# Kernel tuning notes

Hardware: AMD Instinct MI355X
Metric: run time of the kernel (lower is better)

## Reference

```python
import jax, jax.numpy as jnp
import numpy as np

B = 131072
MV_IN, PC_IN, D, OUT = 256, 128, 128, 128
LN_EPS = 1e-5
NORM_EPS = 1e-9


def _lin_init(key, fan_in, fan_out):
    kw, kb = jax.random.split(key)
    s = 1.0 / np.sqrt(fan_in)
    W = jax.random.uniform(kw, (fan_in, fan_out), minval=-s, maxval=s, dtype=jnp.float32)
    b = jax.random.uniform(kb, (fan_out,), minval=-s, maxval=s, dtype=jnp.float32)
    return W, b


def setup_inputs() -> dict:
    key = jax.random.key(0)
    ks = jax.random.split(key, 12)
    mv_enc = jax.random.normal(ks[0], (B, MV_IN), dtype=jnp.float32)
    pc_enc = jax.random.normal(ks[1], (B, PC_IN), dtype=jnp.float32)
    Wq_mv, bq_mv = _lin_init(ks[2], MV_IN, D)
    Wk_mv, bk_mv = _lin_init(ks[3], MV_IN, D)
    Wv_mv, bv_mv = _lin_init(ks[4], MV_IN, D)
    Wq_pc, bq_pc = _lin_init(ks[5], PC_IN, D)
    Wk_pc, bk_pc = _lin_init(ks[6], PC_IN, D)
    Wv_pc, bv_pc = _lin_init(ks[7], PC_IN, D)
    Wq_c, bq_c = _lin_init(ks[8], D, D)
    Wk_c, bk_c = _lin_init(ks[9], D, D)
    Wv_c, bv_c = _lin_init(ks[10], D, D)
    Wp, bp = _lin_init(ks[11], D, OUT)
    ln_g = jnp.ones((OUT,), dtype=jnp.float32)
    ln_b = jnp.zeros((OUT,), dtype=jnp.float32)
    return dict(mv_enc=mv_enc, pc_enc=pc_enc,
                Wq_mv=Wq_mv, bq_mv=bq_mv, Wk_mv=Wk_mv, bk_mv=bk_mv, Wv_mv=Wv_mv, bv_mv=bv_mv,
                Wq_pc=Wq_pc, bq_pc=bq_pc, Wk_pc=Wk_pc, bk_pc=bk_pc, Wv_pc=Wv_pc, bv_pc=bv_pc,
                Wq_c=Wq_c, bq_c=bq_c, Wk_c=Wk_c, bk_c=bk_c, Wv_c=Wv_c, bv_c=bv_c,
                Wp=Wp, bp=bp, ln_g=ln_g, ln_b=ln_b)


def _sa(q, k, v):
    # scaled-dot-product self-attention with residual (+v), seq len = 2
    d = q.shape[-1]
    scores = jnp.einsum('bqd,bkd->bqk', q, k) / jnp.sqrt(jnp.asarray(d, q.dtype))
    a = jax.nn.softmax(scores, axis=-1)
    return jnp.einsum('bqk,bkd->bqd', a, v) + v


def _rep2(t):
    # torch .repeat(1, 2, 1) on a [B,1,D] tensor
    return jnp.concatenate([t, t], axis=1)


def reference(mv_enc, pc_enc,
              Wq_mv, bq_mv, Wk_mv, bk_mv, Wv_mv, bv_mv,
              Wq_pc, bq_pc, Wk_pc, bk_pc, Wv_pc, bv_pc,
              Wq_c, bq_c, Wk_c, bk_c, Wv_c, bv_c,
              Wp, bp, ln_g, ln_b):
    mv = mv_enc[:, None, :]  # [B,1,256]
    pc = pc_enc[:, None, :]  # [B,1,128]
    q_mv = mv @ Wq_mv + bq_mv
    k_mv = mv @ Wk_mv + bk_mv
    v_mv = mv @ Wv_mv + bv_mv
    q_pc = pc @ Wq_pc + bq_pc
    k_pc = pc @ Wk_pc + bk_pc
    v_pc = pc @ Wv_pc + bv_pc
    v_cat = jnp.concatenate([v_mv, v_pc], axis=1)  # [B,2,128]
    res_mv = _sa(_rep2(q_mv), _rep2(k_mv), v_cat).max(axis=1, keepdims=True)  # [B,1,128]
    res_pc = _sa(_rep2(q_pc), _rep2(k_pc), v_cat).max(axis=1, keepdims=True)  # [B,1,128]
    x = jnp.concatenate([res_mv, res_pc], axis=1)  # [B,2,128]
    q_c = x @ Wq_c + bq_c
    k_c = x @ Wk_c + bk_c
    v_c = x @ Wv_c + bv_c
    res = _sa(q_c, k_c, v_c).max(axis=1)  # [B,128]
    h = res @ Wp + bp
    mu = h.mean(axis=-1, keepdims=True)
    var = ((h - mu) ** 2).mean(axis=-1, keepdims=True)
    h = (h - mu) * jax.lax.rsqrt(var + LN_EPS) * ln_g + ln_b
    h = jax.nn.selu(h)
    return h / (jnp.linalg.norm(h, axis=1, keepdims=True) + NORM_EPS)
```

## Files before the change

### kernel.cpp

```cpp
#include <hip/hip_runtime.h>
#include <hip/hip_bf16.h>
#include <math.h>


typedef float f32x4 __attribute__((ext_vector_type(4)));
typedef short s16x8 __attribute__((ext_vector_type(8)));

#define MFMA __builtin_amdgcn_mfma_f32_16x16x32_bf16

__device__ __forceinline__ unsigned short f2bf(float x) {
    __hip_bfloat16 h = __float2bfloat16(x);
    return __builtin_bit_cast(unsigned short, h);
}
__device__ __forceinline__ float bf2f(unsigned short u) {
    return __builtin_bit_cast(float, ((unsigned)u) << 16);
}
__device__ __forceinline__ unsigned packsplit(float x) {
    unsigned short h = f2bf(x);
    unsigned short l = f2bf(x - bf2f(h));
    return ((unsigned)l << 16) | (unsigned)h;
}

__global__ void prep_all(const float* __restrict__ Wv_mv, const float* __restrict__ Wv_pc,
                         const float* __restrict__ Wv_c,  const float* __restrict__ Wp,
                         const float* __restrict__ bv_c,  const float* __restrict__ bp,
                         unsigned short* __restrict__ Fmv, unsigned short* __restrict__ Fpc,
                         unsigned short* __restrict__ Fw2, float* __restrict__ b2) {
    int b = blockIdx.x;
    int l = threadIdx.x;
    if (b < 128) {
        const float* W = nullptr;
        unsigned short* out = nullptr;
        int f;
        bool direct = true;
        if (b < 64)       { W = Wv_mv; out = Fmv; f = b; }
        else if (b < 96)  { W = Wv_pc; out = Fpc; f = b - 64; }
        else              { out = Fw2; f = b - 96; direct = false; }
        int c = f >> 3, t = f & 7;
        int col = t * 16 + (l & 15);
        int k0 = c * 32 + (l >> 4) * 8;
        unsigned short hi[8], lo[8];
        #pragma unroll
        for (int i = 0; i < 8; ++i) {
            float x;
            if (direct) {
                x = W[(size_t)(k0 + i) * 128 + col];
            } else {
                float s = 0.f;
                for (int k = 0; k < 128; ++k)
                    s = fmaf(Wv_c[(size_t)(k0 + i) * 128 + k], Wp[(size_t)k * 128 + col], s);
                x = s;
            }
            unsigned short h = f2bf(x);
            hi[i] = h;
            lo[i] = f2bf(x - bf2f(h));
        }
        unsigned short* base = out + (size_t)f * 1024 + (size_t)l * 8;
        #pragma unroll
        for (int i = 0; i < 8; ++i) base[i] = hi[i];
        #pragma unroll
        for (int i = 0; i < 8; ++i) base[512 + i] = lo[i];
    } else {
        #pragma unroll
        for (int rep = 0; rep < 2; ++rep) {
            int j = l + rep * 64;
            float s = 0.f;
            for (int k = 0; k < 128; ++k) s = fmaf(bv_c[k], Wp[(size_t)k * 128 + j], s);
            b2[j] = 2.f * s + bp[j];
        }
    }
}

__launch_bounds__(256, 3)
__global__ void fused_main(const float* __restrict__ mv, const float* __restrict__ pc,
                           const unsigned short* __restrict__ Fmv,
                           const unsigned short* __restrict__ Fpc,
                           const unsigned short* __restrict__ Fw2,
                           const float* __restrict__ b_mv, const float* __restrict__ b_pc,
                           const float* __restrict__ b2v,
                           const float* __restrict__ ln_g, const float* __restrict__ ln_b,
                           float* __restrict__ out) {
    const int tid = threadIdx.x;
    const int wv  = tid >> 6;
    const int l   = tid & 63;
    const int lg  = l >> 4;
    const int ll  = l & 15;
    const int rowbase = blockIdx.x * 128 + wv * 32;

    const f32x4 vz = {0.f, 0.f, 0.f, 0.f};

    f32x4 acc1[8][2];
    #pragma unroll
    for (int tf = 0; tf < 8; ++tf) { acc1[tf][0] = vz; acc1[tf][1] = vz; }

    #pragma unroll 1
    for (int c = 0; c < 8; ++c) {
        s16x8 dh[2], dl[2];
        #pragma unroll
        for (int ts = 0; ts < 2; ++ts) {
            const float* ap = mv + (size_t)(rowbase + ts * 16 + ll) * 256 + c * 32 + lg * 8;
            f32x4 x0 = *(const f32x4*)ap;
            f32x4 x1 = *(const f32x4*)(ap + 4);
            #pragma unroll
            for (int i = 0; i < 4; ++i) {
                unsigned p0 = packsplit(x0[i]);
                dh[ts][i]     = (short)(p0 & 0xffffu);
                dl[ts][i]     = (short)(p0 >> 16);
                unsigned p1 = packsplit(x1[i]);
                dh[ts][4 + i] = (short)(p1 & 0xffffu);
                dl[ts][4 + i] = (short)(p1 >> 16);
            }
        }
        const unsigned short* fb = Fmv + (size_t)c * 8192 + (size_t)l * 8;
        #pragma unroll
        for (int tf = 0; tf < 8; ++tf) {
            s16x8 wh = *(const s16x8*)(fb + tf * 1024);
            s16x8 wl = *(const s16x8*)(fb + tf * 1024 + 512);
            #pragma unroll
            for (int ts = 0; ts < 2; ++ts) {
                acc1[tf][ts] = MFMA(wh, dh[ts], acc1[tf][ts], 0, 0, 0);
                acc1[tf][ts] = MFMA(wl, dh[ts], acc1[tf][ts], 0, 0, 0);
                acc1[tf][ts] = MFMA(wh, dl[ts], acc1[tf][ts], 0, 0, 0);
            }
        }
    }

    f32x4 acc2[8][2];
    #pragma unroll
    for (int tf = 0; tf < 8; ++tf) { acc2[tf][0] = vz; acc2[tf][1] = vz; }

    #pragma unroll 1
    for (int c = 0; c < 4; ++c) {
        s16x8 dh[2], dl[2];
        #pragma unroll
        for (int ts = 0; ts < 2; ++ts) {
            const float* ap = pc + (size_t)(rowbase + ts * 16 + ll) * 128 + c * 32 + lg * 8;
            f32x4 x0 = *(const f32x4*)ap;
            f32x4 x1 = *(const f32x4*)(ap + 4);
            #pragma unroll
            for (int i = 0; i < 4; ++i) {
                unsigned p0 = packsplit(x0[i]);
                dh[ts][i]     = (short)(p0 & 0xffffu);
                dl[ts][i]     = (short)(p0 >> 16);
                unsigned p1 = packsplit(x1[i]);
                dh[ts][4 + i] = (short)(p1 & 0xffffu);
                dl[ts][4 + i] = (short)(p1 >> 16);
            }
        }
        const unsigned short* fb = Fpc + (size_t)c * 8192 + (size_t)l * 8;
        #pragma unroll
        for (int tf = 0; tf < 8; ++tf) {
            s16x8 wh = *(const s16x8*)(fb + tf * 1024);
            s16x8 wl = *(const s16x8*)(fb + tf * 1024 + 512);
            #pragma unroll
            for (int ts = 0; ts < 2; ++ts) {
                acc2[tf][ts] = MFMA(wh, dh[ts], acc2[tf][ts], 0, 0, 0);
                acc2[tf][ts] = MFMA(wl, dh[ts], acc2[tf][ts], 0, 0, 0);
                acc2[tf][ts] = MFMA(wh, dl[ts], acc2[tf][ts], 0, 0, 0);
            }
        }
    }

    unsigned r2p[8][2][4];
    #pragma unroll
    for (int tf = 0; tf < 8; ++tf) {
        #pragma unroll
        for (int j = 0; j < 4; ++j) {
            float bm = b_mv[tf * 16 + lg * 4 + j];
            float bq = b_pc[tf * 16 + lg * 4 + j];
            #pragma unroll
            for (int ts = 0; ts < 2; ++ts) {
                float x1 = acc1[tf][ts][j] + bm;
                float x2 = acc2[tf][ts][j] + bq;
                float r2 = (x1 + x2) + 2.f * fmaxf(x1, x2);
                r2p[tf][ts][j] = packsplit(r2);
            }
        }
    }

    f32x4 acch[2][8];
    #pragma unroll
    for (int ts = 0; ts < 2; ++ts)
        #pragma unroll
        for (int t = 0; t < 8; ++t) acch[ts][t] = vz;

    const int g0 = (((lg * 2)     ) & 3) * 16 + ll;
    const int g1 = (((lg * 2) + 1 ) & 3) * 16 + ll;
    const bool uhi = (lg & 2) != 0;

    #pragma unroll
    for (int c = 0; c < 4; ++c) {
        s16x8 ah[2], al[2];
        #pragma unroll
        for (int ts = 0; ts < 2; ++ts) {
            #pragma unroll
            for (int q = 0; q < 2; ++q) {
                const int src = q ? g1 : g0;
                #pragma unroll
                for (int j = 0; j < 4; ++j) {
                    unsigned va = __shfl(r2p[2 * c][ts][j], src);
                    unsigned vb = __shfl(r2p[2 * c + 1][ts][j], src);
                    unsigned v  = uhi ? vb : va;
                    ah[ts][q * 4 + j] = (short)(v & 0xffffu);
                    al[ts][q * 4 + j] = (short)(v >> 16);
                }
            }
        }
        const unsigned short* fb = Fw2 + (size_t)c * 8192 + (size_t)l * 8;
        #pragma unroll
        for (int t = 0; t < 8; ++t) {
            s16x8 bh = *(const s16x8*)(fb + t * 1024);
            s16x8 bl = *(const s16x8*)(fb + t * 1024 + 512);
            #pragma unroll
            for (int ts = 0; ts < 2; ++ts) {
                acch[ts][t] = MFMA(ah[ts], bh, acch[ts][t], 0, 0, 0);
                acch[ts][t] = MFMA(al[ts], bh, acch[ts][t], 0, 0, 0);
                acch[ts][t] = MFMA(ah[ts], bl, acch[ts][t], 0, 0, 0);
            }
        }
    }

    float b2c[8], bg[8], bb[8];
    #pragma unroll
    for (int t = 0; t < 8; ++t) {
        b2c[t] = b2v[t * 16 + ll];
        bg[t]  = ln_g[t * 16 + ll];
        bb[t]  = ln_b[t * 16 + ll];
    }
    #pragma unroll
    for (int ts = 0; ts < 2; ++ts) {
        #pragma unroll
        for (int j = 0; j < 4; ++j) {
            float v[8];
            float sum = 0.f, ssq = 0.f;
            #pragma unroll
            for (int t = 0; t < 8; ++t) {
                float h = acch[ts][t][j] + b2c[t];
                v[t] = h;
                sum += h;
                ssq = fmaf(h, h, ssq);
            }
            #pragma unroll
            for (int o = 1; o < 16; o <<= 1) {
                sum += __shfl_xor(sum, o);
                ssq += __shfl_xor(ssq, o);
            }
            float mu  = sum * 0.0078125f;
            float var = ssq * 0.0078125f - mu * mu;
            float rs  = 1.f / sqrtf(var + 1e-5f);
            float s2  = 0.f;
            #pragma unroll
            for (int t = 0; t < 8; ++t) {
                float hn = (v[t] - mu) * rs * bg[t] + bb[t];
                float m  = hn > 0.f ? hn : 1.6732632423543772f * expm1f(hn);
                m = 1.0507009873554805f * m;
                v[t] = m;
                s2 = fmaf(m, m, s2);
            }
            #pragma unroll
            for (int o = 1; o < 16; o <<= 1) s2 += __shfl_xor(s2, o);
            float sc = 1.f / (sqrtf(s2) + 1e-9f);
            int row = rowbase + ts * 16 + lg * 4 + j;
            float* op = out + (size_t)row * 128 + ll;
            #pragma unroll
            for (int t = 0; t < 8; ++t) op[t * 16] = v[t] * sc;
        }
    }
}

extern "C" void kernel_launch(void* const* d_in, const int* in_sizes, int n_in,
                              void* d_out, int out_size, void* d_ws, size_t ws_size,
                              hipStream_t stream) {
    const float* mv    = (const float*)d_in[0];
    const float* pc    = (const float*)d_in[1];
    const float* Wv_mv = (const float*)d_in[6];
    const float* bv_mv = (const float*)d_in[7];
    const float* Wv_pc = (const float*)d_in[12];
    const float* bv_pc = (const float*)d_in[13];
    const float* Wv_c  = (const float*)d_in[18];
    const float* bv_c  = (const float*)d_in[19];
    const float* Wp    = (const float*)d_in[20];
    const float* bp    = (const float*)d_in[21];
    const float* ln_g  = (const float*)d_in[22];
    const float* ln_b  = (const float*)d_in[23];
    float* out = (float*)d_out;

    char* ws = (char*)d_ws;
    unsigned short* Fmv = (unsigned short*)ws;
    unsigned short* Fpc = Fmv + 65536;
    unsigned short* Fw2 = Fpc + 32768;
    float* b2 = (float*)(ws + 262144);

    prep_all<<<129, 64, 0, stream>>>(Wv_mv, Wv_pc, Wv_c, Wp, bv_c, bp,
                                     Fmv, Fpc, Fw2, b2);
    fused_main<<<1024, 256, 0, stream>>>(mv, pc, Fmv, Fpc, Fw2,
                                         bv_mv, bv_pc, b2, ln_g, ln_b, out);
}
```

Before: 403.1 us.

## Halve rows per wave, move r2 transpose to swizzled LDS, raise occupancy

Each wave now handles 16 rows instead of 32, which halves the accumulator register footprint. Launch bounds go from 3 to 4 blocks and the grid doubles. The intermediate r2 transpose between the first and second GEMM stage now goes through XOR-swizzled shared memory instead of many cross-lane shuffles, and MFMA operand order is swapped so the accumulator layout matches. The cost is that each weight fragment loaded from global/L2 now feeds half as many MFMAs, which doubles weight traffic per row, and an added block-level barrier.

```diff
diff --git a/kernel.cpp b/kernel.cpp
--- a/kernel.cpp
+++ b/kernel.cpp
@@ -4,6 +4,7 @@
 
 
 typedef float f32x4 __attribute__((ext_vector_type(4)));
+typedef unsigned u32x4 __attribute__((ext_vector_type(4)));
 typedef short s16x8 __attribute__((ext_vector_type(8)));
 
 #define MFMA __builtin_amdgcn_mfma_f32_16x16x32_bf16
@@ -71,7 +72,7 @@
     }
 }
 
-__launch_bounds__(256, 3)
+__launch_bounds__(256, 4)
 __global__ void fused_main(const float* __restrict__ mv, const float* __restrict__ pc,
                            const unsigned short* __restrict__ Fmv,
                            const unsigned short* __restrict__ Fpc,
@@ -80,143 +81,118 @@
                            const float* __restrict__ b2v,
                            const float* __restrict__ ln_g, const float* __restrict__ ln_b,
                            float* __restrict__ out) {
+    __shared__ unsigned r2lds[4][2048];
     const int tid = threadIdx.x;
     const int wv  = tid >> 6;
     const int l   = tid & 63;
     const int lg  = l >> 4;
     const int ll  = l & 15;
-    const int rowbase = blockIdx.x * 128 + wv * 32;
+    const int rowbase = blockIdx.x * 64 + wv * 16;
 
     const f32x4 vz = {0.f, 0.f, 0.f, 0.f};
 
-    f32x4 acc1[8][2];
-    #pragma unroll
-    for (int tf = 0; tf < 8; ++tf) { acc1[tf][0] = vz; acc1[tf][1] = vz; }
-
-    #pragma unroll 1
+    f32x4 acc1[8];
+    #pragma unroll
+    for (int tf = 0; tf < 8; ++tf) acc1[tf] = vz;
+
+    #pragma unroll 2
     for (int c = 0; c < 8; ++c) {
-        s16x8 dh[2], dl[2];
-        #pragma unroll
-        for (int ts = 0; ts < 2; ++ts) {
-            const float* ap = mv + (size_t)(rowbase + ts * 16 + ll) * 256 + c * 32 + lg * 8;
-            f32x4 x0 = *(const f32x4*)ap;
-            f32x4 x1 = *(const f32x4*)(ap + 4);
-            #pragma unroll
-            for (int i = 0; i < 4; ++i) {
-                unsigned p0 = packsplit(x0[i]);
-                dh[ts][i]     = (short)(p0 & 0xffffu);
-                dl[ts][i]     = (short)(p0 >> 16);
-                unsigned p1 = packsplit(x1[i]);
-                dh[ts][4 + i] = (short)(p1 & 0xffffu);
-                dl[ts][4 + i] = (short)(p1 >> 16);
-            }
+        const float* ap = mv + (size_t)(rowbase + ll) * 256 + c * 32 + lg * 8;
+        f32x4 x0 = *(const f32x4*)ap;
+        f32x4 x1 = *(const f32x4*)(ap + 4);
+        s16x8 dh, dl;
+        #pragma unroll
+        for (int i = 0; i < 4; ++i) {
+            unsigned p0 = packsplit(x0[i]);
+            dh[i]     = (short)(p0 & 0xffffu);
+            dl[i]     = (short)(p0 >> 16);
+            unsigned p1 = packsplit(x1[i]);
+            dh[4 + i] = (short)(p1 & 0xffffu);
+            dl[4 + i] = (short)(p1 >> 16);
         }
         const unsigned short* fb = Fmv + (size_t)c * 8192 + (size_t)l * 8;
         #pragma unroll
         for (int tf = 0; tf < 8; ++tf) {
             s16x8 wh = *(const s16x8*)(fb + tf * 1024);
             s16x8 wl = *(const s16x8*)(fb + tf * 1024 + 512);
-            #pragma unroll
-            for (int ts = 0; ts < 2; ++ts) {
-                acc1[tf][ts] = MFMA(wh, dh[ts], acc1[tf][ts], 0, 0, 0);
-                acc1[tf][ts] = MFMA(wl, dh[ts], acc1[tf][ts], 0, 0, 0);
-                acc1[tf][ts] = MFMA(wh, dl[ts], acc1[tf][ts], 0, 0, 0);
-            }
-        }
-    }
-
-    f32x4 acc2[8][2];
-    #pragma unroll
-    for (int tf = 0; tf < 8; ++tf) { acc2[tf][0] = vz; acc2[tf][1] = vz; }
-
-    #pragma unroll 1
+            acc1[tf] = MFMA(dh, wh, acc1[tf], 0, 0, 0);
+            acc1[tf] = MFMA(dl, wh, acc1[tf], 0, 0, 0);
+            acc1[tf] = MFMA(dh, wl, acc1[tf], 0, 0, 0);
+        }
+    }
+
+    f32x4 acc2[8];
+    #pragma unroll
+    for (int tf = 0; tf < 8; ++tf) acc2[tf] = vz;
+
+    #pragma unroll 2
     for (int c = 0; c < 4; ++c) {
-        s16x8 dh[2], dl[2];
-        #pragma unroll
-        for (int ts = 0; ts < 2; ++ts) {
-            const float* ap = pc + (size_t)(rowbase + ts * 16 + ll) * 128 + c * 32 + lg * 8;
-            f32x4 x0 = *(const f32x4*)ap;
-            f32x4 x1 = *(const f32x4*)(ap + 4);
-            #pragma unroll
-            for (int i = 0; i < 4; ++i) {
-                unsigned p0 = packsplit(x0[i]);
-                dh[ts][i]     = (short)(p0 & 0xffffu);
-                dl[ts][i]     = (short)(p0 >> 16);
-                unsigned p1 = packsplit(x1[i]);
-                dh[ts][4 + i] = (short)(p1 & 0xffffu);
-                dl[ts][4 + i] = (short)(p1 >> 16);
-            }
+        const float* ap = pc + (size_t)(rowbase + ll) * 128 + c * 32 + lg * 8;
+        f32x4 x0 = *(const f32x4*)ap;
+        f32x4 x1 = *(const f32x4*)(ap + 4);
+        s16x8 dh, dl;
+        #pragma unroll
+        for (int i = 0; i < 4; ++i) {
+            unsigned p0 = packsplit(x0[i]);
+            dh[i]     = (short)(p0 & 0xffffu);
+            dl[i]     = (short)(p0 >> 16);
+            unsigned p1 = packsplit(x1[i]);
+            dh[4 + i] = (short)(p1 & 0xffffu);
+            dl[4 + i] = (short)(p1 >> 16);
         }
         const unsigned short* fb = Fpc + (size_t)c * 8192 + (size_t)l * 8;
         #pragma unroll
         for (int tf = 0; tf < 8; ++tf) {
             s16x8 wh = *(const s16x8*)(fb + tf * 1024);
             s16x8 wl = *(const s16x8*)(fb + tf * 1024 + 512);
+            acc2[tf] = MFMA(dh, wh, acc2[tf], 0, 0, 0);
+            acc2[tf] = MFMA(dl, wh, acc2[tf], 0, 0, 0);
+            acc2[tf] = MFMA(dh, wl, acc2[tf], 0, 0, 0);
+        }
+    }
+
+    unsigned* base = &r2lds[wv][0];
+    #pragma unroll
+    for (int tf = 0; tf < 8; ++tf) {
+        float bm = b_mv[tf * 16 + ll];
+        float bq = b_pc[tf * 16 + ll];
+        #pragma unroll
+        for (int j = 0; j < 4; ++j) {
+            int row = lg * 4 + j;
+            float x1 = acc1[tf][j] + bm;
+            float x2 = acc2[tf][j] + bq;
+            float r2 = (x1 + x2) + 2.f * fmaxf(x1, x2);
+            int dw = row * 128 + tf * 16 + ll;
+            base[dw ^ ((row & 7) << 2)] = packsplit(r2);
+        }
+    }
+    __syncthreads();
+
+    f32x4 acch[8];
+    #pragma unroll
+    for (int t = 0; t < 8; ++t) acch[t] = vz;
+
+    #pragma unroll
+    for (int c = 0; c < 4; ++c) {
+        s16x8 ah, al;
+        #pragma unroll
+        for (int q = 0; q < 2; ++q) {
+            int dw = ll * 128 + c * 32 + lg * 8 + q * 4;
+            u32x4 u = *(const u32x4*)&base[dw ^ ((ll & 7) << 2)];
             #pragma unroll
-            for (int ts = 0; ts < 2; ++ts) {
-                acc2[tf][ts] = MFMA(wh, dh[ts], acc2[tf][ts], 0, 0, 0);
-                acc2[tf][ts] = MFMA(wl, dh[ts], acc2[tf][ts], 0, 0, 0);
-                acc2[tf][ts] = MFMA(wh, dl[ts], acc2[tf][ts], 0, 0, 0);
+            for (int j = 0; j < 4; ++j) {
+                ah[q * 4 + j] = (short)(u[j] & 0xffffu);
+                al[q * 4 + j] = (short)(u[j] >> 16);
             }
         }
-    }
-
-    unsigned r2p[8][2][4];
-    #pragma unroll
-    for (int tf = 0; tf < 8; ++tf) {
-        #pragma unroll
-        for (int j = 0; j < 4; ++j) {
-            float bm = b_mv[tf * 16 + lg * 4 + j];
-            float bq = b_pc[tf * 16 + lg * 4 + j];
-            #pragma unroll
-            for (int ts = 0; ts < 2; ++ts) {
-                float x1 = acc1[tf][ts][j] + bm;
-                float x2 = acc2[tf][ts][j] + bq;
-                float r2 = (x1 + x2) + 2.f * fmaxf(x1, x2);
-                r2p[tf][ts][j] = packsplit(r2);
-            }
-        }
-    }
-
-    f32x4 acch[2][8];
-    #pragma unroll
-    for (int ts = 0; ts < 2; ++ts)
-        #pragma unroll
-        for (int t = 0; t < 8; ++t) acch[ts][t] = vz;
-
-    const int g0 = (((lg * 2)     ) & 3) * 16 + ll;
-    const int g1 = (((lg * 2) + 1 ) & 3) * 16 + ll;
-    const bool uhi = (lg & 2) != 0;
-
-    #pragma unroll
-    for (int c = 0; c < 4; ++c) {
-        s16x8 ah[2], al[2];
-        #pragma unroll
-        for (int ts = 0; ts < 2; ++ts) {
-            #pragma unroll
-            for (int q = 0; q < 2; ++q) {
-                const int src = q ? g1 : g0;
-                #pragma unroll
-                for (int j = 0; j < 4; ++j) {
-                    unsigned va = __shfl(r2p[2 * c][ts][j], src);
-                    unsigned vb = __shfl(r2p[2 * c + 1][ts][j], src);
-                    unsigned v  = uhi ? vb : va;
-                    ah[ts][q * 4 + j] = (short)(v & 0xffffu);
-                    al[ts][q * 4 + j] = (short)(v >> 16);
-                }
-            }
-        }
         const unsigned short* fb = Fw2 + (size_t)c * 8192 + (size_t)l * 8;
         #pragma unroll
         for (int t = 0; t < 8; ++t) {
-            s16x8 bh = *(const s16x8*)(fb + t * 1024);
-            s16x8 bl = *(const s16x8*)(fb + t * 1024 + 512);
-            #pragma unroll
-            for (int ts = 0; ts < 2; ++ts) {
-                acch[ts][t] = MFMA(ah[ts], bh, acch[ts][t], 0, 0, 0);
-                acch[ts][t] = MFMA(al[ts], bh, acch[ts][t], 0, 0, 0);
-                acch[ts][t] = MFMA(ah[ts], bl, acch[ts][t], 0, 0, 0);
-            }
+            s16x8 wh = *(const s16x8*)(fb + t * 1024);
+            s16x8 wl = *(const s16x8*)(fb + t * 1024 + 512);
+            acch[t] = MFMA(ah, wh, acch[t], 0, 0, 0);
+            acch[t] = MFMA(al, wh, acch[t], 0, 0, 0);
+            acch[t] = MFMA(ah, wl, acch[t], 0, 0, 0);
         }
     }
 
@@ -228,43 +204,40 @@
         bb[t]  = ln_b[t * 16 + ll];
     }
     #pragma unroll
-    for (int ts = 0; ts < 2; ++ts) {
-        #pragma unroll
-        for (int j = 0; j < 4; ++j) {
-            float v[8];
-            float sum = 0.f, ssq = 0.f;
-            #pragma unroll
-            for (int t = 0; t < 8; ++t) {
-                float h = acch[ts][t][j] + b2c[t];
-                v[t] = h;
-                sum += h;
-                ssq = fmaf(h, h, ssq);
-            }
-            #pragma unroll
-            for (int o = 1; o < 16; o <<= 1) {
-                sum += __shfl_xor(sum, o);
-                ssq += __shfl_xor(ssq, o);
-            }
-            float mu  = sum * 0.0078125f;
-            float var = ssq * 0.0078125f - mu * mu;
-            float rs  = 1.f / sqrtf(var + 1e-5f);
-            float s2  = 0.f;
-            #pragma unroll
-            for (int t = 0; t < 8; ++t) {
-                float hn = (v[t] - mu) * rs * bg[t] + bb[t];
-                float m  = hn > 0.f ? hn : 1.6732632423543772f * expm1f(hn);
-                m = 1.0507009873554805f * m;
-                v[t] = m;
-                s2 = fmaf(m, m, s2);
-            }
-            #pragma unroll
-            for (int o = 1; o < 16; o <<= 1) s2 += __shfl_xor(s2, o);
-            float sc = 1.f / (sqrtf(s2) + 1e-9f);
-            int row = rowbase + ts * 16 + lg * 4 + j;
-            float* op = out + (size_t)row * 128 + ll;
-            #pragma unroll
-            for (int t = 0; t < 8; ++t) op[t * 16] = v[t] * sc;
-        }
+    for (int j = 0; j < 4; ++j) {
+        float v[8];
+        float sum = 0.f, ssq = 0.f;
+        #pragma unroll
+        for (int t = 0; t < 8; ++t) {
+            float h = acch[t][j] + b2c[t];
+            v[t] = h;
+            sum += h;
+            ssq = fmaf(h, h, ssq);
+        }
+        #pragma unroll
+        for (int o = 1; o < 16; o <<= 1) {
+            sum += __shfl_xor(sum, o);
+            ssq += __shfl_xor(ssq, o);
+        }
+        float mu  = sum * 0.0078125f;
+        float var = ssq * 0.0078125f - mu * mu;
+        float rs  = 1.f / sqrtf(var + 1e-5f);
+        float s2  = 0.f;
+        #pragma unroll
+        for (int t = 0; t < 8; ++t) {
+            float hn = (v[t] - mu) * rs * bg[t] + bb[t];
+            float m  = hn > 0.f ? hn : 1.6732632423543772f * expm1f(hn);
+            m = 1.0507009873554805f * m;
+            v[t] = m;
+            s2 = fmaf(m, m, s2);
+        }
+        #pragma unroll
+        for (int o = 1; o < 16; o <<= 1) s2 += __shfl_xor(s2, o);
+        float sc = 1.f / (sqrtf(s2) + 1e-9f);
+        int row = rowbase + lg * 4 + j;
+        float* op = out + (size_t)row * 128 + ll;
+        #pragma unroll
+        for (int t = 0; t < 8; ++t) op[t * 16] = v[t] * sc;
     }
 }
 
@@ -293,6 +266,6 @@
 
     prep_all<<<129, 64, 0, stream>>>(Wv_mv, Wv_pc, Wv_c, Wp, bv_c, bp,
                                      Fmv, Fpc, Fw2, b2);
-    fused_main<<<1024, 256, 0, stream>>>(mv, pc, Fmv, Fpc, Fw2,
+    fused_main<<<2048, 256, 0, stream>>>(mv, pc, Fmv, Fpc, Fw2,
                                          bv_mv, bv_pc, b2, ln_g, ln_b, out);
 }
```

New measurement: 381.3 us. 1.06x faster.
